# Kernel optimization log

Measured on AMD Instinct MI355X. Metric: run time of the kernel, lower is better.

## Reference

```python
import jax, jax.numpy as jnp
import numpy as np

N_NODES = 100000
IN_CH = 256
OUT_CH = 128
N_EDGES = 3200000
SCALING_FACTOR = 1.8


def gcn_propagate(x, edge_index, num_nodes):
    """APPNP(K=1, alpha=0) == one step of D^-1/2 (A+I) D^-1/2 @ x."""
    row, col = edge_index[0], edge_index[1]
    loops = jnp.arange(num_nodes, dtype=edge_index.dtype)
    row = jnp.concatenate([row, loops])
    col = jnp.concatenate([col, loops])
    ones = jnp.ones(row.shape[0], dtype=x.dtype)
    deg = jax.ops.segment_sum(ones, col, num_segments=num_nodes)  # [N]
    dinv = jnp.where(deg > 0, jax.lax.rsqrt(deg), 0.0)
    norm = dinv[row] * dinv[col]  # [E+N]
    msgs = x[row] * norm[:, None]  # gather + scale, [E+N, C]
    return jax.ops.segment_sum(msgs, col, num_segments=num_nodes)  # [N, C]


def setup_inputs() -> dict:
    key = jax.random.key(0)
    ks = jax.random.split(key, 7)
    x = jax.random.normal(ks[0], (N_NODES, IN_CH), dtype=jnp.float32)
    edge_index = jax.random.randint(ks[1], (2, N_EDGES), 0, N_NODES, dtype=jnp.int64)
    s1 = 1.0 / np.sqrt(IN_CH)
    W1 = jax.random.uniform(ks[2], (IN_CH, OUT_CH), jnp.float32, -s1, s1)
    b1 = jax.random.uniform(ks[3], (OUT_CH,), jnp.float32, -s1, s1)
    W2 = jax.random.uniform(ks[4], (IN_CH, OUT_CH), jnp.float32, -s1, s1)
    b2 = jax.random.uniform(ks[5], (OUT_CH,), jnp.float32, -s1, s1)
    return {"x": x, "edge_index": edge_index, "W1": W1, "b1": b1, "W2": W2, "b2": b2}


def reference(x, edge_index, W1, b1, W2, b2):
    num_nodes = x.shape[0]
    # branch 1: linear1 then propagate
    x_ = x @ W1 + b1
    x_ = gcn_propagate(x_, edge_index, num_nodes)
    # branch 2: linear2, L2 normalize per-row, scale, then propagate
    h = x @ W2 + b2
    nrm = jnp.sqrt(jnp.sum(h * h, axis=1, keepdims=True))
    h = h / jnp.maximum(nrm, 1e-12) * SCALING_FACTOR
    h = gcn_propagate(h, edge_index, num_nodes)
    return (h, x_)
```

## Files before the change

kernel.cpp:

```cpp
#include <hip/hip_runtime.h>

#define IN_CH   256
#define OUT_CH  128
#define SCALE   1.8f
#define GT_M    64
#define BKT_SH  8
#define BKT_CAP 9216

using bf16x8 = __attribute__((ext_vector_type(8))) short;
using f32x4  = __attribute__((ext_vector_type(4))) float;

__device__ __forceinline__ float blo(unsigned int w) { return __uint_as_float(w << 16); }
__device__ __forceinline__ float bhi(unsigned int w) { return __uint_as_float(w & 0xffff0000u); }
__device__ __forceinline__ unsigned short f2b(float f) {
    unsigned int u = __float_as_uint(f);
    u += 0x7fffu + ((u >> 16) & 1u);
    return (unsigned short)(u >> 16);
}
__device__ __forceinline__ void split2(float f, unsigned short& h, unsigned short& l) {
    h = f2b(f);
    float hf = __uint_as_float((unsigned int)h << 16);
    l = f2b(f - hf);
}

__global__ __launch_bounds__(256) void wsplit_kernel(const float* __restrict__ W1, const float* __restrict__ b1,
                                                     const float* __restrict__ W2, const float* __restrict__ b2,
                                                     unsigned short* __restrict__ Wfh, unsigned short* __restrict__ Wfl,
                                                     float* __restrict__ bc, int* __restrict__ bktCur) {
    int n = blockIdx.x;
    int k = threadIdx.x;
    if (n < 2) {
        int i = n * 256 + k;
        bktCur[i] = i * BKT_CAP;
    }
    float w = (n < OUT_CH) ? W2[k * OUT_CH + n] : W1[k * OUT_CH + (n - OUT_CH)];
    unsigned short h, l;
    split2(w, h, l);
    int idx = (((k >> 5) * 16 + (n >> 4)) * 64 + ((k >> 3) & 3) * 16 + (n & 15)) * 8 + (k & 7);
    Wfh[idx] = h;
    Wfl[idx] = l;
    if (k == 0) bc[n] = (n < OUT_CH) ? b2[n] : b1[n - OUT_CH];
}

__device__ __forceinline__ void part_body(char* smem, const int* __restrict__ row, const int* __restrict__ col,
                                          int* __restrict__ bktCur, unsigned int* __restrict__ pairs,
                                          int E, int NBKT, int nPart, int pb) {
    int* lh   = (int*)smem;
    int* lcur = lh + 512;
    int t = threadIdx.x;
    lh[t] = 0; lh[t + 256] = 0;
    __syncthreads();
    int tile = (E + nPart - 1) / nPart;
    int e0 = pb * tile;
    int e1 = min(E, e0 + tile);
    if ((tile & 3) == 0 && (e0 & 3) == 0 && e1 == e0 + tile) {
        const uint4* c4 = (const uint4*)(col + e0);
        const uint4* r4 = (const uint4*)(row + e0);
        int n4 = tile >> 2;
        for (int i = t; i < n4; i += 256) {
            uint4 c = c4[i];
            atomicAdd(&lh[c.x >> BKT_SH], 1);
            atomicAdd(&lh[c.y >> BKT_SH], 1);
            atomicAdd(&lh[c.z >> BKT_SH], 1);
            atomicAdd(&lh[c.w >> BKT_SH], 1);
        }
        __syncthreads();
        for (int b = t; b < 512; b += 256) {
            int c = (b < NBKT) ? lh[b] : 0;
            lcur[b] = (c > 0) ? atomicAdd(&bktCur[b], c) : 0;
        }
        __syncthreads();
        for (int i = t; i < n4; i += 256) {
            uint4 c = c4[i];
            uint4 r = r4[i];
            int p0 = atomicAdd(&lcur[c.x >> BKT_SH], 1); pairs[p0] = ((c.x & 255u) << 17) | r.x;
            int p1 = atomicAdd(&lcur[c.y >> BKT_SH], 1); pairs[p1] = ((c.y & 255u) << 17) | r.y;
            int p2 = atomicAdd(&lcur[c.z >> BKT_SH], 1); pairs[p2] = ((c.z & 255u) << 17) | r.z;
            int p3 = atomicAdd(&lcur[c.w >> BKT_SH], 1); pairs[p3] = ((c.w & 255u) << 17) | r.w;
        }
    } else {
        for (int i = e0 + t; i < e1; i += 256)
            atomicAdd(&lh[col[i] >> BKT_SH], 1);
        __syncthreads();
        for (int b = t; b < 512; b += 256) {
            int c = (b < NBKT) ? lh[b] : 0;
            lcur[b] = (c > 0) ? atomicAdd(&bktCur[b], c) : 0;
        }
        __syncthreads();
        for (int i = e0 + t; i < e1; i += 256) {
            int c = col[i];
            int pos = atomicAdd(&lcur[c >> BKT_SH], 1);
            pairs[pos] = ((unsigned int)(c & 255) << 17) | (unsigned int)row[i];
        }
    }
}

__device__ __forceinline__ void csr_body(char* smem, const unsigned int* __restrict__ pairs,
                                         const int* __restrict__ bktCur,
                                         int* __restrict__ csr, int* __restrict__ offs,
                                         int* __restrict__ deg, float* __restrict__ dinv,
                                         int N, int b) {
    int* s    = (int*)smem;
    int* nc   = (int*)(smem + 1024);
    int* ncur = (int*)(smem + 2048);
    int t = threadIdx.x;
    int base = b * BKT_CAP;
    int cnt = bktCur[b] - base;

    nc[t] = 0;
    __syncthreads();
    for (int i = t; i < cnt; i += 256)
        atomicAdd(&nc[pairs[base + i] >> 17], 1);
    __syncthreads();
    int dv = nc[t];
    s[t] = dv;
    __syncthreads();
    for (int o = 1; o < 256; o <<= 1) {
        int u = (t >= o) ? s[t - o] : 0;
        __syncthreads();
        s[t] += u;
        __syncthreads();
    }
    int rel = s[t] - dv;
    int n = (b << BKT_SH) + t;
    if (n < N) {
        offs[n] = base + rel;
        deg[n] = dv;
        dinv[n] = 1.0f / sqrtf((float)dv + 1.0f);
    }
    ncur[t] = rel;
    __syncthreads();
    for (int i = t; i < cnt; i += 256) {
        unsigned int k = pairs[base + i];
        int node = k >> 17;
        int pos = atomicAdd(&ncur[node], 1);
        csr[base + pos] = (int)(k & 0x1FFFF);
    }
}

#define XPAD 264
#define GEMM_SMEM (GT_M * XPAD * 2 + 2 * GT_M * 4)
__device__ __forceinline__ void gemm_body(char* smem, const float* __restrict__ x,
                                          const unsigned short* __restrict__ Wfh,
                                          const unsigned short* __restrict__ Wfl,
                                          const float* __restrict__ bc,
                                          unsigned short* __restrict__ gb, int blockRow, int N) {
    unsigned short* xh = (unsigned short*)smem;
    float* sn = (float*)(smem + GT_M * XPAD * sizeof(unsigned short));

    int t = threadIdx.x;
    size_t row0 = (size_t)blockRow * GT_M;

    const float4* xg = (const float4*)(x + row0 * IN_CH);
#pragma unroll
    for (int i = 0; i < 16; i++) {
        int f4 = t + i * 256;
        int row = f4 >> 6;
        int c4 = (f4 & 63) * 4;
        uint2 hw = {0u, 0u};
        if (row0 + row < (size_t)N) {
            float4 v = xg[f4];
            hw.x = (unsigned int)f2b(v.x) | ((unsigned int)f2b(v.y) << 16);
            hw.y = (unsigned int)f2b(v.z) | ((unsigned int)f2b(v.w) << 16);
        }
        *(uint2*)&xh[row * XPAD + c4] = hw;
    }
    __syncthreads();

    int lane = t & 63;
    int wv = t >> 6;
    int lr = lane & 15;
    int lk = (lane >> 4) * 8;

    f32x4 acc[4][4];
#pragma unroll
    for (int rt = 0; rt < 4; rt++)
#pragma unroll
        for (int ct = 0; ct < 4; ct++) acc[rt][ct] = (f32x4){0.f, 0.f, 0.f, 0.f};

#pragma unroll
    for (int kt = 0; kt < 8; kt++) {
        int k0 = kt * 32;
        bf16x8 bh[4], bl[4];
#pragma unroll
        for (int ct = 0; ct < 4; ct++) {
            int fidx = ((kt * 16 + wv * 4 + ct) * 64 + lane) * 8;
            bh[ct] = *(const bf16x8*)&Wfh[fidx];
            bl[ct] = *(const bf16x8*)&Wfl[fidx];
        }
        bf16x8 ah[4];
#pragma unroll
        for (int rt = 0; rt < 4; rt++) {
            int idx = (rt * 16 + lr) * XPAD + k0 + lk;
            ah[rt] = *(const bf16x8*)&xh[idx];
        }
#pragma unroll
        for (int rt = 0; rt < 4; rt++)
#pragma unroll
            for (int ct = 0; ct < 4; ct++) {
                acc[rt][ct] = __builtin_amdgcn_mfma_f32_16x16x32_bf16(ah[rt], bh[ct], acc[rt][ct], 0, 0, 0);
                acc[rt][ct] = __builtin_amdgcn_mfma_f32_16x16x32_bf16(ah[rt], bl[ct], acc[rt][ct], 0, 0, 0);
            }
    }
    __syncthreads();

    float bcv[4];
#pragma unroll
    for (int ct = 0; ct < 4; ct++) bcv[ct] = bc[wv * 64 + ct * 16 + lr];
#pragma unroll
    for (int rt = 0; rt < 4; rt++)
#pragma unroll
        for (int ct = 0; ct < 4; ct++)
#pragma unroll
            for (int j = 0; j < 4; j++) acc[rt][ct][j] += bcv[ct];

    if (wv < 2) {
        float nr[4][4];
#pragma unroll
        for (int rt = 0; rt < 4; rt++)
#pragma unroll
            for (int j = 0; j < 4; j++) {
                float sum = 0.f;
#pragma unroll
                for (int ct = 0; ct < 4; ct++) sum += acc[rt][ct][j] * acc[rt][ct][j];
                nr[rt][j] = sum;
            }
#pragma unroll
        for (int o = 1; o < 16; o <<= 1)
#pragma unroll
            for (int rt = 0; rt < 4; rt++)
#pragma unroll
                for (int j = 0; j < 4; j++) nr[rt][j] += __shfl_xor(nr[rt][j], o);
        if (lr == 0) {
#pragma unroll
            for (int rt = 0; rt < 4; rt++)
#pragma unroll
                for (int j = 0; j < 4; j++)
                    sn[wv * GT_M + rt * 16 + (lane >> 4) * 4 + j] = nr[rt][j];
        }
    }
    __syncthreads();

#pragma unroll
    for (int rt = 0; rt < 4; rt++) {
#pragma unroll
        for (int j = 0; j < 4; j++) {
            int rl = rt * 16 + (lane >> 4) * 4 + j;
            if (row0 + rl >= (size_t)N) continue;
            float sf;
            if (wv < 2) {
                float n2 = sn[rl] + sn[GT_M + rl];
                sf = SCALE / fmaxf(sqrtf(n2), 1e-12f);
            } else {
                sf = 1.0f;
            }
            size_t base = (row0 + rl) * 256;
#pragma unroll
            for (int ct = 0; ct < 4; ct++) {
                int col = wv * 64 + ct * 16 + lr;
                gb[base + col] = f2b(acc[rt][ct][j] * sf);
            }
        }
    }
}

__global__ __launch_bounds__(256) void k1_part_gemm(const int* __restrict__ row, const int* __restrict__ col,
                                                    int* __restrict__ bktCur, unsigned int* __restrict__ pairs,
                                                    int E, int NBKT, int nPart,
                                                    const float* __restrict__ x,
                                                    const unsigned short* __restrict__ Wfh,
                                                    const unsigned short* __restrict__ Wfl,
                                                    const float* __restrict__ bc,
                                                    unsigned short* __restrict__ gb, int N) {
    __shared__ __align__(16) char smem[GEMM_SMEM];
    int b = (int)blockIdx.x;
    if (b < nPart) part_body(smem, row, col, bktCur, pairs, E, NBKT, nPart, b);
    else gemm_body(smem, x, Wfh, Wfl, bc, gb, b - nPart, N);
}

__global__ __launch_bounds__(256) void k2_csr_gemm(const unsigned int* __restrict__ pairs,
                                                   const int* __restrict__ bktCur,
                                                   int* __restrict__ csr, int* __restrict__ offs,
                                                   int* __restrict__ deg, float* __restrict__ dinv,
                                                   int N, int nCsr, int gemmRowBase,
                                                   const float* __restrict__ x,
                                                   const unsigned short* __restrict__ Wfh,
                                                   const unsigned short* __restrict__ Wfl,
                                                   const float* __restrict__ bc,
                                                   unsigned short* __restrict__ gb) {
    __shared__ __align__(16) char smem[GEMM_SMEM];
    int b = (int)blockIdx.x;
    if (b < nCsr) csr_body(smem, pairs, bktCur, csr, offs, deg, dinv, N, b);
    else gemm_body(smem, x, Wfh, Wfl, bc, gb, gemmRowBase + (b - nCsr), N);
}

__global__ __launch_bounds__(256) void gather_kernel(const uint4* __restrict__ gp,
                                                     const int* __restrict__ offs, const int* __restrict__ deg,
                                                     const int* __restrict__ csr, const float* __restrict__ dinv,
                                                     float* __restrict__ outh, float* __restrict__ outx,
                                                     int n0, int n1) {
    int t = threadIdx.x;
    int n = n0 + (blockIdx.x << 2) + (t >> 6);
    if (n >= n1) return;
    int l = t & 63;
    int half = l >> 5;
    int cl = l & 31;

    float a0 = 0.f, a1 = 0.f, a2 = 0.f, a3 = 0.f, a4 = 0.f, a5 = 0.f, a6 = 0.f, a7 = 0.f;
    auto accumw = [&](uint4 w, float ds) {
        a0 += blo(w.x) * ds; a1 += bhi(w.x) * ds;
        a2 += blo(w.y) * ds; a3 += bhi(w.y) * ds;
        a4 += blo(w.z) * ds; a5 += bhi(w.z) * ds;
        a6 += blo(w.w) * ds; a7 += bhi(w.w) * ds;
    };

    float dn = dinv[n];
    if (half == 0) accumw(gp[(size_t)n * 32 + cl], dn);

    int s0 = offs[n];
    int e1 = s0 + deg[n];
    int e = s0 + half;
    for (; e + 2 < e1; e += 4) {
        int sa = csr[e];
        int sb = csr[e + 2];
        float da = dinv[sa];
        float db = dinv[sb];
        uint4 wa = gp[(size_t)sa * 32 + cl];
        uint4 wb = gp[(size_t)sb * 32 + cl];
        accumw(wa, da); accumw(wb, db);
    }
    for (; e < e1; e += 2) {
        int sa = csr[e];
        accumw(gp[(size_t)sa * 32 + cl], dinv[sa]);
    }

    a0 += __shfl_xor(a0, 32);
    a1 += __shfl_xor(a1, 32);
    a2 += __shfl_xor(a2, 32);
    a3 += __shfl_xor(a3, 32);
    a4 += __shfl_xor(a4, 32);
    a5 += __shfl_xor(a5, 32);
    a6 += __shfl_xor(a6, 32);
    a7 += __shfl_xor(a7, 32);

    if (half == 0) {
        float4 v0 = {a0 * dn, a1 * dn, a2 * dn, a3 * dn};
        float4 v1 = {a4 * dn, a5 * dn, a6 * dn, a7 * dn};
        if (cl < 16) {
            float* o = &outh[(size_t)n * OUT_CH + cl * 8];
            *(float4*)o = v0;
            *(float4*)(o + 4) = v1;
        } else {
            float* o = &outx[(size_t)n * OUT_CH + (cl - 16) * 8];
            *(float4*)o = v0;
            *(float4*)(o + 4) = v1;
        }
    }
}

extern "C" void kernel_launch(void* const* d_in, const int* in_sizes, int n_in,
                              void* d_out, int out_size, void* d_ws, size_t ws_size,
                              hipStream_t stream) {
    const float* x   = (const float*)d_in[0];
    const int*   ei  = (const int*)d_in[1];
    const float* W1  = (const float*)d_in[2];
    const float* b1  = (const float*)d_in[3];
    const float* W2  = (const float*)d_in[4];
    const float* b2  = (const float*)d_in[5];

    const int N = in_sizes[0] / IN_CH;
    const int E = in_sizes[1] / 2;
    const int NBKT = (N + 255) >> BKT_SH;

    float* outh = (float*)d_out;
    float* outx = outh + (size_t)N * OUT_CH;

    char* p = (char*)d_ws;
    auto take = [&](size_t bytes) {
        char* q = p;
        p += (bytes + 255) & ~(size_t)255;
        return q;
    };
    int*   deg     = (int*)take((size_t)N * sizeof(int));
    float* dinv    = (float*)take((size_t)N * sizeof(float));
    int*   offs    = (int*)take((size_t)N * sizeof(int));
    int*   bktCur  = (int*)take(512 * sizeof(int));
    float* bc      = (float*)take(256 * sizeof(float));
    unsigned short* Wfh = (unsigned short*)take(256 * 256 * sizeof(unsigned short));
    unsigned short* Wfl = (unsigned short*)take(256 * 256 * sizeof(unsigned short));
    int*   csr     = (int*)take((size_t)NBKT * BKT_CAP * sizeof(int));
    unsigned int* pairs = (unsigned int*)take((size_t)NBKT * BKT_CAP * sizeof(unsigned int));
    unsigned short* gb = (unsigned short*)take((size_t)N * 256 * sizeof(unsigned short));

    const int* erow = ei;
    const int* ecol = ei + E;

    const int nPart = 1000;
    const int gemmBlocks = (N + GT_M - 1) / GT_M;
    const int gemmA = (gemmBlocks + 1) / 2;
    const int gemmB = gemmBlocks - gemmA;

    wsplit_kernel<<<256, 256, 0, stream>>>(W1, b1, W2, b2, Wfh, Wfl, bc, bktCur);
    k1_part_gemm<<<nPart + gemmA, 256, 0, stream>>>(erow, ecol, bktCur, pairs, E, NBKT, nPart,
                                                    x, Wfh, Wfl, bc, gb, N);
    k2_csr_gemm<<<NBKT + gemmB, 256, 0, stream>>>(pairs, bktCur, csr, offs, deg, dinv, N, NBKT, gemmA,
                                                  x, Wfh, Wfl, bc, gb);

    int c1 = (N + 2) / 3;
    int c2 = 2 * c1;
    gather_kernel<<<(c1 + 3) / 4, 256, 0, stream>>>((const uint4*)gb, offs, deg, csr, dinv, outh, outx, 0, c1);
    gather_kernel<<<(c1 + 3) / 4, 256, 0, stream>>>((const uint4*)gb, offs, deg, csr, dinv, outh, outx, c1, c2);
    gather_kernel<<<(N - c2 + 3) / 4, 256, 0, stream>>>((const uint4*)gb, offs, deg, csr, dinv, outh, outx, c2, N);
}
```

Measured before the change: 400.6 us.

## Split fused partition/CSR/GEMM kernels into separate launches and merge gather launches

Undoes the co-scheduling of edge partitioning and CSR building with halves of the GEMM inside shared kernels, and launches partition, CSR, GEMM and gather as separate kernels. Each kernel now has its own shared memory footprint, so the small partition and CSR kernels no longer reserve the large GEMM buffer, which may raise their occupancy. The three gather launches become one, and the partition block count is halved. The cost is losing the overlap of the irregular graph preprocessing with the dense GEMM.

After: 393.0 us. About the same (-1.9%).

```diff
diff --git a/kernel.cpp b/kernel.cpp
--- a/kernel.cpp
+++ b/kernel.cpp
@@ -42,11 +42,12 @@
     if (k == 0) bc[n] = (n < OUT_CH) ? b2[n] : b1[n - OUT_CH];
 }
 
-__device__ __forceinline__ void part_body(char* smem, const int* __restrict__ row, const int* __restrict__ col,
-                                          int* __restrict__ bktCur, unsigned int* __restrict__ pairs,
-                                          int E, int NBKT, int nPart, int pb) {
-    int* lh   = (int*)smem;
-    int* lcur = lh + 512;
+__global__ __launch_bounds__(256) void part_kernel(const int* __restrict__ row, const int* __restrict__ col,
+                                                   int* __restrict__ bktCur, unsigned int* __restrict__ pairs,
+                                                   int E, int NBKT, int nPart) {
+    __shared__ int lh[512];
+    __shared__ int lcur[512];
+    int pb = (int)blockIdx.x;
     int t = threadIdx.x;
     lh[t] = 0; lh[t + 256] = 0;
     __syncthreads();
@@ -95,14 +96,15 @@
     }
 }
 
-__device__ __forceinline__ void csr_body(char* smem, const unsigned int* __restrict__ pairs,
-                                         const int* __restrict__ bktCur,
-                                         int* __restrict__ csr, int* __restrict__ offs,
-                                         int* __restrict__ deg, float* __restrict__ dinv,
-                                         int N, int b) {
-    int* s    = (int*)smem;
-    int* nc   = (int*)(smem + 1024);
-    int* ncur = (int*)(smem + 2048);
+__global__ __launch_bounds__(256) void csr_kernel(const unsigned int* __restrict__ pairs,
+                                                  const int* __restrict__ bktCur,
+                                                  int* __restrict__ csr, int* __restrict__ offs,
+                                                  int* __restrict__ deg, float* __restrict__ dinv,
+                                                  int N) {
+    __shared__ int s[256];
+    __shared__ int nc[256];
+    __shared__ int ncur[256];
+    int b = (int)blockIdx.x;
     int t = threadIdx.x;
     int base = b * BKT_CAP;
     int cnt = bktCur[b] - base;
@@ -139,17 +141,16 @@
 }
 
 #define XPAD 264
-#define GEMM_SMEM (GT_M * XPAD * 2 + 2 * GT_M * 4)
-__device__ __forceinline__ void gemm_body(char* smem, const float* __restrict__ x,
-                                          const unsigned short* __restrict__ Wfh,
-                                          const unsigned short* __restrict__ Wfl,
-                                          const float* __restrict__ bc,
-                                          unsigned short* __restrict__ gb, int blockRow, int N) {
-    unsigned short* xh = (unsigned short*)smem;
-    float* sn = (float*)(smem + GT_M * XPAD * sizeof(unsigned short));
+__global__ __launch_bounds__(256) void gemm_kernel(const float* __restrict__ x,
+                                                   const unsigned short* __restrict__ Wfh,
+                                                   const unsigned short* __restrict__ Wfl,
+                                                   const float* __restrict__ bc,
+                                                   unsigned short* __restrict__ gb, int N) {
+    __shared__ unsigned short xh[GT_M * XPAD];
+    __shared__ float sn[2 * GT_M];
 
     int t = threadIdx.x;
-    size_t row0 = (size_t)blockRow * GT_M;
+    size_t row0 = (size_t)blockIdx.x * GT_M;
 
     const float4* xg = (const float4*)(x + row0 * IN_CH);
 #pragma unroll
@@ -264,44 +265,13 @@
     }
 }
 
-__global__ __launch_bounds__(256) void k1_part_gemm(const int* __restrict__ row, const int* __restrict__ col,
-                                                    int* __restrict__ bktCur, unsigned int* __restrict__ pairs,
-                                                    int E, int NBKT, int nPart,
-                                                    const float* __restrict__ x,
-                                                    const unsigned short* __restrict__ Wfh,
-                                                    const unsigned short* __restrict__ Wfl,
-                                                    const float* __restrict__ bc,
-                                                    unsigned short* __restrict__ gb, int N) {
-    __shared__ __align__(16) char smem[GEMM_SMEM];
-    int b = (int)blockIdx.x;
-    if (b < nPart) part_body(smem, row, col, bktCur, pairs, E, NBKT, nPart, b);
-    else gemm_body(smem, x, Wfh, Wfl, bc, gb, b - nPart, N);
-}
-
-__global__ __launch_bounds__(256) void k2_csr_gemm(const unsigned int* __restrict__ pairs,
-                                                   const int* __restrict__ bktCur,
-                                                   int* __restrict__ csr, int* __restrict__ offs,
-                                                   int* __restrict__ deg, float* __restrict__ dinv,
-                                                   int N, int nCsr, int gemmRowBase,
-                                                   const float* __restrict__ x,
-                                                   const unsigned short* __restrict__ Wfh,
-                                                   const unsigned short* __restrict__ Wfl,
-                                                   const float* __restrict__ bc,
-                                                   unsigned short* __restrict__ gb) {
-    __shared__ __align__(16) char smem[GEMM_SMEM];
-    int b = (int)blockIdx.x;
-    if (b < nCsr) csr_body(smem, pairs, bktCur, csr, offs, deg, dinv, N, b);
-    else gemm_body(smem, x, Wfh, Wfl, bc, gb, gemmRowBase + (b - nCsr), N);
-}
-
 __global__ __launch_bounds__(256) void gather_kernel(const uint4* __restrict__ gp,
                                                      const int* __restrict__ offs, const int* __restrict__ deg,
                                                      const int* __restrict__ csr, const float* __restrict__ dinv,
-                                                     float* __restrict__ outh, float* __restrict__ outx,
-                                                     int n0, int n1) {
+                                                     float* __restrict__ outh, float* __restrict__ outx, int N) {
     int t = threadIdx.x;
-    int n = n0 + (blockIdx.x << 2) + (t >> 6);
-    if (n >= n1) return;
+    int n = (blockIdx.x << 2) + (t >> 6);
+    if (n >= N) return;
     int l = t & 63;
     int half = l >> 5;
     int cl = l & 31;
@@ -395,20 +365,11 @@
     const int* erow = ei;
     const int* ecol = ei + E;
 
-    const int nPart = 1000;
-    const int gemmBlocks = (N + GT_M - 1) / GT_M;
-    const int gemmA = (gemmBlocks + 1) / 2;
-    const int gemmB = gemmBlocks - gemmA;
+    const int nPart = 500;
 
     wsplit_kernel<<<256, 256, 0, stream>>>(W1, b1, W2, b2, Wfh, Wfl, bc, bktCur);
-    k1_part_gemm<<<nPart + gemmA, 256, 0, stream>>>(erow, ecol, bktCur, pairs, E, NBKT, nPart,
-                                                    x, Wfh, Wfl, bc, gb, N);
-    k2_csr_gemm<<<NBKT + gemmB, 256, 0, stream>>>(pairs, bktCur, csr, offs, deg, dinv, N, NBKT, gemmA,
-                                                  x, Wfh, Wfl, bc, gb);
-
-    int c1 = (N + 2) / 3;
-    int c2 = 2 * c1;
-    gather_kernel<<<(c1 + 3) / 4, 256, 0, stream>>>((const uint4*)gb, offs, deg, csr, dinv, outh, outx, 0, c1);
-    gather_kernel<<<(c1 + 3) / 4, 256, 0, stream>>>((const uint4*)gb, offs, deg, csr, dinv, outh, outx, c1, c2);
-    gather_kernel<<<(N - c2 + 3) / 4, 256, 0, stream>>>((const uint4*)gb, offs, deg, csr, dinv, outh, outx, c2, N);
-}
+    part_kernel<<<nPart, 256, 0, stream>>>(erow, ecol, bktCur, pairs, E, NBKT, nPart);
+    csr_kernel<<<NBKT, 256, 0, stream>>>(pairs, bktCur, csr, offs, deg, dinv, N);
+    gemm_kernel<<<(N + GT_M - 1) / GT_M, 256, 0, stream>>>(x, Wfh, Wfl, bc, gb, N);
+    gather_kernel<<<(N + 3) / 4, 256, 0, stream>>>((const uint4*)gb, offs, deg, csr, dinv, outh, outx, N);
+}
```
